# Optimization experiments

Hardware: AMD Instinct MI355X
Metric: run time of the kernel (lower is better)

Reference implementation:

```python
import jax, jax.numpy as jnp
import numpy as np

N = 10000      # nodes
DEG = 32       # avg degree
D_IN = 256     # in_feats
H = 128        # hidden_layers[0] == hidden_layers[2]
K = 3          # hidden_layers[1] = Chebyshev order
D_OUT = 64     # out_feat


def setup_inputs() -> dict:
    key = jax.random.key(0)
    ks = jax.random.split(key, 8)
    x = jax.random.normal(ks[0], (N, D_IN), jnp.float32)
    # sparse binary adjacency built by scattering into a dense [N, N] matrix
    src = jax.random.randint(ks[1], (N * DEG,), 0, N)
    dst = jax.random.randint(ks[2], (N * DEG,), 0, N)
    adj = jnp.zeros((N, N), jnp.float32).at[src, dst].set(1.0)
    init = lambda k, shape, fan: jax.random.normal(k, shape, jnp.float32) / np.sqrt(fan)
    W_in = init(ks[3], (D_IN, H), D_IN)
    b_in = jnp.zeros((H,), jnp.float32)
    W_cheb = init(ks[4], (K * H, H), K * H)   # dgl ChebConv: Linear(k*in, out)
    b_cheb = jnp.zeros((H,), jnp.float32)
    W_out = init(ks[5], (H, D_OUT), H)
    b_out = jnp.zeros((D_OUT,), jnp.float32)
    return dict(x=x, adj=adj, W_in=W_in, b_in=b_in, W_cheb=W_cheb,
                b_cheb=b_cheb, W_out=W_out, b_out=b_out)


def reference(x, adj, W_in, b_in, W_cheb, b_cheb, W_out, b_out):
    n = x.shape[0]
    # graph construction from dense adjacency (eager, like adj.to_dense().nonzero())
    src, dst = jnp.nonzero(adj)
    # symmetric normalization on in-degrees (dgl ChebConv, norm clamped at 1)
    deg = jax.ops.segment_sum(jnp.ones(src.shape[0], jnp.float32), dst, num_segments=n)
    norm = jnp.clip(deg, 1.0) ** -0.5  # [n]
    re_norm = 2.0 / 2.0  # lambda_max = [2] -> re_norm = 1

    def prop(h):
        # D^{-1/2} A D^{-1/2} h : gather at src, scatter-add at dst
        return jax.ops.segment_sum((h * norm[:, None])[src], dst, num_segments=n) * norm[:, None]

    # input linear + relu
    h = jax.nn.relu(x @ W_in + b_in)
    # Chebyshev recursion (dgl ChebConv with lambda_max=2)
    X0 = h
    X1 = -re_norm * prop(X0) + (re_norm - 1.0) * X0
    Xs = [X0, X1]
    Xpp, Xp = X0, X1
    for _ in range(2, K):
        Xi = -2.0 * re_norm * prop(Xp) + 2.0 * (re_norm - 1.0) * Xp - Xpp
        Xs.append(Xi)
        Xpp, Xp = Xp, Xi
    hc = jax.nn.relu(jnp.concatenate(Xs, axis=1) @ W_cheb + b_cheb)  # [n, H]
    return hc @ W_out + b_out  # [n, D_OUT]
```

## Files before the change

### kernel.cpp

```cpp
#include <hip/hip_runtime.h>
#include <hip/hip_bf16.h>
#include <cstdint>
#include <cstddef>

#define NN 10000
#define MAXDEG 128
#define LDX 384

#define GEMM_BLKS 313
#define CONV_BLK  1
#define SCAN_BLKS 3072
#define FAT_BLKS  (GEMM_BLKS + CONV_BLK + SCAN_BLKS)

typedef __attribute__((ext_vector_type(8))) short bf16x8;
typedef __attribute__((ext_vector_type(4))) float f32x4;

__device__ __forceinline__ float bf2f(unsigned short u) {
    union { unsigned int i; float f; } c; c.i = ((unsigned int)u) << 16; return c.f;
}
__device__ __forceinline__ unsigned short f2bf(float f) {
    union { float f; unsigned int i; } c; c.f = f;
    unsigned int x = c.i;
    return (unsigned short)((x + 0x7fffu + ((x >> 16) & 1u)) >> 16);
}

__global__ __launch_bounds__(256) void fat_scan_gemm(
        const float4* __restrict__ adj4, int total4,
        int* __restrict__ cnt, int* __restrict__ csr,
        const float* __restrict__ x, const float* __restrict__ W_in,
        const float* __restrict__ b_in,
        const float* __restrict__ W_cheb, const float* __restrict__ W_out,
        unsigned short* __restrict__ Xc,
        unsigned short* __restrict__ Wtc, unsigned short* __restrict__ Wto) {
    __shared__ float smem[10240];
    int bid = blockIdx.x;
    int t = threadIdx.x;

    if (bid < GEMM_BLKS) {
        constexpr int K = 256, N = 128, BM = 32, KC = 64;
        float* Wl = smem;
        float* Al = smem + KC * N;
        int r0 = bid * BM;
        int c2 = t & 63;
        int g  = t >> 6;
        float2 acc[8];
        #pragma unroll
        for (int i = 0; i < 8; ++i) acc[i] = make_float2(0.f, 0.f);

        for (int kk = 0; kk < K; kk += KC) {
            __syncthreads();
            #pragma unroll
            for (int i = 0; i < KC * N / 4 / 256; ++i) {
                int idx = t + i * 256;
                ((float4*)Wl)[idx] = ((const float4*)(W_in + (size_t)kk * N))[idx];
            }
            #pragma unroll
            for (int i = 0; i < BM * KC / 4 / 256; ++i) {
                int idx = t + i * 256;
                int row = idx >> 4;
                int cf  = idx & 15;
                float4 v = make_float4(0.f, 0.f, 0.f, 0.f);
                if (r0 + row < NN)
                    v = *(const float4*)(x + (size_t)(r0 + row) * K + kk + cf * 4);
                *(float4*)(Al + row * KC + cf * 4) = v;
            }
            __syncthreads();
            for (int k = 0; k < KC; k += 4) {
                float4 av[8];
                #pragma unroll
                for (int rr = 0; rr < 8; ++rr)
                    av[rr] = *(const float4*)(Al + (g * 8 + rr) * KC + k);
                #pragma unroll
                for (int k2 = 0; k2 < 4; ++k2) {
                    float2 wv = *(const float2*)(Wl + (k + k2) * N + c2 * 2);
                    #pragma unroll
                    for (int rr = 0; rr < 8; ++rr) {
                        float a = (k2 == 0) ? av[rr].x : (k2 == 1) ? av[rr].y
                                  : (k2 == 2) ? av[rr].z : av[rr].w;
                        acc[rr].x = fmaf(a, wv.x, acc[rr].x);
                        acc[rr].y = fmaf(a, wv.y, acc[rr].y);
                    }
                }
            }
        }
        float2 bv = *(const float2*)(b_in + c2 * 2);
        #pragma unroll
        for (int rr = 0; rr < 8; ++rr) {
            int r = r0 + g * 8 + rr;
            if (r < NN) {
                float vx = fmaxf(acc[rr].x + bv.x, 0.f);
                float vy = fmaxf(acc[rr].y + bv.y, 0.f);
                uint32_t o = (uint32_t)f2bf(vx) | ((uint32_t)f2bf(vy) << 16);
                *(uint32_t*)(Xc + (size_t)r * LDX + c2 * 2) = o;
            }
        }
    } else if (bid == GEMM_BLKS) {
        for (int idx = t; idx < 384 * 128; idx += 256) {
            int k = idx >> 7, c = idx & 127;
            Wtc[c * 384 + k] = f2bf(W_cheb[idx]);
        }
        for (int idx = t; idx < 128 * 64; idx += 256) {
            int k = idx >> 6, c = idx & 63;
            Wto[c * 128 + k] = f2bf(W_out[idx]);
        }
    } else {
        int sid = bid - (GEMM_BLKS + CONV_BLK);
        int idx = sid * 256 + t;
        int stride = SCAN_BLKS * 256;
        for (int p = idx; p < total4; p += stride) {
            float4 v = adj4[p];
            if (v.x != 0.f || v.y != 0.f || v.z != 0.f || v.w != 0.f) {
                int lin = p * 4;
                #pragma unroll
                for (int c = 0; c < 4; ++c) {
                    float f = (c == 0) ? v.x : (c == 1) ? v.y : (c == 2) ? v.z : v.w;
                    if (f != 0.f) {
                        int l = lin + c;
                        int i = l / NN;
                        int j = l - i * NN;
                        int pos = atomicAdd(&cnt[j], 1);
                        if (pos < MAXDEG) csr[j * MAXDEG + pos] = i;
                    }
                }
            }
        }
    }
}

template<bool SUB>
__global__ __launch_bounds__(256) void prop_k(unsigned short* __restrict__ X,
                                              const int* __restrict__ csr,
                                              const int* __restrict__ cnt,
                                              int srcOff, int dstOff, float scale) {
    int j = blockIdx.x * 4 + (threadIdx.x >> 6);
    if (j >= NN) return;
    int lane = threadIdx.x & 63;
    int cj = cnt[j];
    int cn = min(cj, MAXDEG);
    const int* nb = csr + j * MAXDEG;
    float ax0 = 0.f, ay0 = 0.f, ax1 = 0.f, ay1 = 0.f;
    int e = 0;
    for (; e + 2 <= cn; e += 2) {
        int i0 = nb[e], i1 = nb[e + 1];
        int c0 = cnt[i0], c1 = cnt[i1];
        uint32_t h0 = *(const uint32_t*)(X + (size_t)i0 * LDX + srcOff + lane * 2);
        uint32_t h1 = *(const uint32_t*)(X + (size_t)i1 * LDX + srcOff + lane * 2);
        float w0 = rsqrtf(fmaxf((float)c0, 1.f));
        float w1 = rsqrtf(fmaxf((float)c1, 1.f));
        ax0 = fmaf(w0, bf2f((unsigned short)h0), ax0);
        ay0 = fmaf(w0, bf2f((unsigned short)(h0 >> 16)), ay0);
        ax1 = fmaf(w1, bf2f((unsigned short)h1), ax1);
        ay1 = fmaf(w1, bf2f((unsigned short)(h1 >> 16)), ay1);
    }
    if (e < cn) {
        int i0 = nb[e];
        float w0 = rsqrtf(fmaxf((float)cnt[i0], 1.f));
        uint32_t h0 = *(const uint32_t*)(X + (size_t)i0 * LDX + srcOff + lane * 2);
        ax0 = fmaf(w0, bf2f((unsigned short)h0), ax0);
        ay0 = fmaf(w0, bf2f((unsigned short)(h0 >> 16)), ay0);
    }
    float s = scale * rsqrtf(fmaxf((float)cj, 1.f));
    float rx = s * (ax0 + ax1), ry = s * (ay0 + ay1);
    if (SUB) {
        uint32_t x0 = *(const uint32_t*)(X + (size_t)j * LDX + lane * 2);
        rx -= bf2f((unsigned short)x0);
        ry -= bf2f((unsigned short)(x0 >> 16));
    }
    uint32_t o = (uint32_t)f2bf(rx) | ((uint32_t)f2bf(ry) << 16);
    *(uint32_t*)(X + (size_t)j * LDX + dstOff + lane * 2) = o;
}

__global__ __launch_bounds__(256) void cheb_out_mfma(
        const unsigned short* __restrict__ Xc,
        const unsigned short* __restrict__ Wtc,
        const float* __restrict__ bc,
        const unsigned short* __restrict__ Wto,
        const float* __restrict__ bo,
        float* __restrict__ out) {
    __shared__ unsigned short hcL[32][136];
    int t = threadIdx.x;
    int w = t >> 6, lane = t & 63;
    int r0 = blockIdx.x * 32;
    int lr = lane & 15;
    int kg = lane >> 4;

    f32x4 acc[2][2] = {};
    for (int k0 = 0; k0 < 384; k0 += 32) {
        bf16x8 a[2], b[2];
        #pragma unroll
        for (int m = 0; m < 2; ++m) {
            int row = r0 + m * 16 + lr;
            row = min(row, NN - 1);
            a[m] = *(const bf16x8*)(Xc + (size_t)row * LDX + k0 + kg * 8);
        }
        #pragma unroll
        for (int n = 0; n < 2; ++n) {
            int col = w * 32 + n * 16 + lr;
            b[n] = *(const bf16x8*)(Wtc + (size_t)col * 384 + k0 + kg * 8);
        }
        #pragma unroll
        for (int m = 0; m < 2; ++m)
            #pragma unroll
            for (int n = 0; n < 2; ++n)
                acc[m][n] = __builtin_amdgcn_mfma_f32_16x16x32_bf16(a[m], b[n], acc[m][n], 0, 0, 0);
    }
    #pragma unroll
    for (int m = 0; m < 2; ++m) {
        #pragma unroll
        for (int n = 0; n < 2; ++n) {
            int col = w * 32 + n * 16 + lr;
            float bv = bc[col];
            #pragma unroll
            for (int r = 0; r < 4; ++r) {
                int row = m * 16 + kg * 4 + r;
                hcL[row][col] = f2bf(fmaxf(acc[m][n][r] + bv, 0.f));
            }
        }
    }
    __syncthreads();
    int rt = w >> 1, ch = w & 1;
    f32x4 a2[2] = {};
    for (int k0 = 0; k0 < 128; k0 += 32) {
        bf16x8 af = *(const bf16x8*)(&hcL[rt * 16 + lr][k0 + kg * 8]);
        #pragma unroll
        for (int n = 0; n < 2; ++n) {
            int col = ch * 32 + n * 16 + lr;
            bf16x8 bf_ = *(const bf16x8*)(Wto + (size_t)col * 128 + k0 + kg * 8);
            a2[n] = __builtin_amdgcn_mfma_f32_16x16x32_bf16(af, bf_, a2[n], 0, 0, 0);
        }
    }
    #pragma unroll
    for (int n = 0; n < 2; ++n) {
        int col = ch * 32 + n * 16 + lr;
        float bv = bo[col];
        #pragma unroll
        for (int r = 0; r < 4; ++r) {
            int row = r0 + rt * 16 + kg * 4 + r;
            if (row < NN) out[(size_t)row * 64 + col] = a2[n][r] + bv;
        }
    }
}

extern "C" void kernel_launch(void* const* d_in, const int* in_sizes, int n_in,
                              void* d_out, int out_size, void* d_ws, size_t ws_size,
                              hipStream_t stream) {
    const float* x      = (const float*)d_in[0];
    const float* adj    = (const float*)d_in[1];
    const float* W_in   = (const float*)d_in[2];
    const float* b_in   = (const float*)d_in[3];
    const float* W_cheb = (const float*)d_in[4];
    const float* b_cheb = (const float*)d_in[5];
    const float* W_out  = (const float*)d_in[6];
    const float* b_out  = (const float*)d_in[7];
    float* out = (float*)d_out;

    char* ws = (char*)d_ws;
    int*            cnt = (int*)(ws + 0);
    int*            csr = (int*)(ws + 40960);
    unsigned short* Xc  = (unsigned short*)(ws + 5160960);
    unsigned short* Wtc = (unsigned short*)(ws + 12845056);
    unsigned short* Wto = (unsigned short*)(ws + 12943360);

    int adj_total = in_sizes[1];

    hipMemsetAsync(cnt, 0, NN * sizeof(int), stream);
    fat_scan_gemm<<<FAT_BLKS, 256, 0, stream>>>(
        (const float4*)adj, adj_total / 4, cnt, csr,
        x, W_in, b_in, W_cheb, W_out, Xc, Wtc, Wto);
    prop_k<false><<<(NN + 3) / 4, 256, 0, stream>>>(Xc, csr, cnt, 0, 128, -1.0f);
    prop_k<true><<<(NN + 3) / 4, 256, 0, stream>>>(Xc, csr, cnt, 128, 256, -2.0f);
    cheb_out_mfma<<<(NN + 31) / 32, 256, 0, stream>>>(Xc, Wtc, b_cheb, Wto, b_out, out);
}
```

Before: 238.5 us.

## Replace atomic adjacency scan with column-blocked scan plus prefix-sum stitch

The dense adjacency is now scanned in 80-row by 4-column tiles. Each thread records nonzero row indices into fixed-size per-segment buckets with no atomics, so the global atomicAdd per edge and the memset are gone. A new stitch kernel prefix-sums the per-block counts with wave shuffles, writes an ordered CSR, and precomputes the rsqrt degree norms. prop_k then reads those norms instead of recomputing them from counts, and is unrolled to 4 neighbours per step. The cost is an extra kernel launch and intermediate buffers. Segments are capped at 12 entries, so a column with more than 12 nonzeros inside one 80-row block silently drops edges.

```diff
diff --git a/kernel.cpp b/kernel.cpp
--- a/kernel.cpp
+++ b/kernel.cpp
@@ -7,10 +7,12 @@
 #define MAXDEG 128
 #define LDX 384
 
+#define COLSCAN_BLKS 1250
+#define RB_ROWS 80
+#define NRB 125
+#define SEG2 12
 #define GEMM_BLKS 313
-#define CONV_BLK  1
-#define SCAN_BLKS 3072
-#define FAT_BLKS  (GEMM_BLKS + CONV_BLK + SCAN_BLKS)
+#define FATG (COLSCAN_BLKS + GEMM_BLKS + 1)
 
 typedef __attribute__((ext_vector_type(8))) short bf16x8;
 typedef __attribute__((ext_vector_type(4))) float f32x4;
@@ -24,23 +26,55 @@
     return (unsigned short)((x + 0x7fffu + ((x >> 16) & 1u)) >> 16);
 }
 
-__global__ __launch_bounds__(256) void fat_scan_gemm(
-        const float4* __restrict__ adj4, int total4,
-        int* __restrict__ cnt, int* __restrict__ csr,
+__global__ __launch_bounds__(256) void fat_colscan_gemm(
+        const float* __restrict__ A,
+        int* __restrict__ csr2,
+        int* __restrict__ cnt2,
         const float* __restrict__ x, const float* __restrict__ W_in,
         const float* __restrict__ b_in,
         const float* __restrict__ W_cheb, const float* __restrict__ W_out,
         unsigned short* __restrict__ Xc,
         unsigned short* __restrict__ Wtc, unsigned short* __restrict__ Wto) {
-    __shared__ float smem[10240];
+    __shared__ float smem[5120];
     int bid = blockIdx.x;
     int t = threadIdx.x;
 
-    if (bid < GEMM_BLKS) {
-        constexpr int K = 256, N = 128, BM = 32, KC = 64;
+    if (bid < COLSCAN_BLKS) {
+        if (t >= 250) return;
+        int rb  = bid / 10;
+        int cbs = bid % 10;
+        int r0  = rb * RB_ROWS;
+        int c   = cbs * 1000 + t * 4;
+        const float4* base = (const float4*)A;
+        int idx0 = r0 * (NN / 4) + (c >> 2);
+
+        float4 buf[8];
+        #pragma unroll
+        for (int d = 0; d < 8; ++d)
+            buf[d] = base[idx0 + d * (NN / 4)];
+
+        int n0 = 0, n1 = 0, n2 = 0, n3 = 0;
+        size_t segbase = ((size_t)rb * NN + c) * SEG2;
+
+        #pragma unroll 8
+        for (int r = 0; r < RB_ROWS; ++r) {
+            float4 v = buf[r & 7];
+            buf[r & 7] = base[idx0 + min(r + 8, RB_ROWS - 1) * (NN / 4)];
+            int row = r0 + r;
+            if (v.x != 0.f) { if (n0 < SEG2) csr2[segbase + n0] = row; n0++; }
+            if (v.y != 0.f) { if (n1 < SEG2) csr2[segbase + SEG2 + n1] = row; n1++; }
+            if (v.z != 0.f) { if (n2 < SEG2) csr2[segbase + 2 * SEG2 + n2] = row; n2++; }
+            if (v.w != 0.f) { if (n3 < SEG2) csr2[segbase + 3 * SEG2 + n3] = row; n3++; }
+        }
+        cnt2[(c + 0) * 128 + rb] = n0;
+        cnt2[(c + 1) * 128 + rb] = n1;
+        cnt2[(c + 2) * 128 + rb] = n2;
+        cnt2[(c + 3) * 128 + rb] = n3;
+    } else if (bid < COLSCAN_BLKS + GEMM_BLKS) {
+        constexpr int K = 256, N = 128, BM = 32, KC = 32;
         float* Wl = smem;
         float* Al = smem + KC * N;
-        int r0 = bid * BM;
+        int r0 = (bid - COLSCAN_BLKS) * BM;
         int c2 = t & 63;
         int g  = t >> 6;
         float2 acc[8];
@@ -54,11 +88,9 @@
                 int idx = t + i * 256;
                 ((float4*)Wl)[idx] = ((const float4*)(W_in + (size_t)kk * N))[idx];
             }
-            #pragma unroll
-            for (int i = 0; i < BM * KC / 4 / 256; ++i) {
-                int idx = t + i * 256;
-                int row = idx >> 4;
-                int cf  = idx & 15;
+            {
+                int row = t >> 3;
+                int cf  = t & 7;
                 float4 v = make_float4(0.f, 0.f, 0.f, 0.f);
                 if (r0 + row < NN)
                     v = *(const float4*)(x + (size_t)(r0 + row) * K + kk + cf * 4);
@@ -94,7 +126,7 @@
                 *(uint32_t*)(Xc + (size_t)r * LDX + c2 * 2) = o;
             }
         }
-    } else if (bid == GEMM_BLKS) {
+    } else {
         for (int idx = t; idx < 384 * 128; idx += 256) {
             int k = idx >> 7, c = idx & 127;
             Wtc[c * 384 + k] = f2bf(W_cheb[idx]);
@@ -103,27 +135,46 @@
             int k = idx >> 6, c = idx & 63;
             Wto[c * 128 + k] = f2bf(W_out[idx]);
         }
-    } else {
-        int sid = bid - (GEMM_BLKS + CONV_BLK);
-        int idx = sid * 256 + t;
-        int stride = SCAN_BLKS * 256;
-        for (int p = idx; p < total4; p += stride) {
-            float4 v = adj4[p];
-            if (v.x != 0.f || v.y != 0.f || v.z != 0.f || v.w != 0.f) {
-                int lin = p * 4;
-                #pragma unroll
-                for (int c = 0; c < 4; ++c) {
-                    float f = (c == 0) ? v.x : (c == 1) ? v.y : (c == 2) ? v.z : v.w;
-                    if (f != 0.f) {
-                        int l = lin + c;
-                        int i = l / NN;
-                        int j = l - i * NN;
-                        int pos = atomicAdd(&cnt[j], 1);
-                        if (pos < MAXDEG) csr[j * MAXDEG + pos] = i;
-                    }
-                }
-            }
-        }
+    }
+}
+
+__global__ __launch_bounds__(256) void stitch_norm(
+        const int* __restrict__ csr2, const int* __restrict__ cnt2,
+        int* __restrict__ csr, int* __restrict__ cnt, float* __restrict__ nrm) {
+    int w = threadIdx.x >> 6, l = threadIdx.x & 63;
+    int c = blockIdx.x * 4 + w;
+    if (c >= NN) return;
+
+    int a  = (l < NRB)      ? cnt2[c * 128 + l]      : 0;
+    int bb = (l + 64 < NRB) ? cnt2[c * 128 + 64 + l] : 0;
+
+    int xa = a, xb = bb;
+    #pragma unroll
+    for (int d = 1; d < 64; d <<= 1) {
+        int ya = __shfl_up(xa, d);
+        int yb = __shfl_up(xb, d);
+        if (l >= d) { xa += ya; xb += yb; }
+    }
+    int totalA = __shfl(xa, 63);
+    int total  = totalA + __shfl(xb, 63);
+    int offA = xa - a;
+    int offB = totalA + xb - bb;
+
+    const int* segA = csr2 + ((size_t)l * NN + c) * SEG2;
+    for (int e = 0; e < a; ++e) {
+        int o = offA + e;
+        if (o < MAXDEG) csr[(size_t)c * MAXDEG + o] = segA[e];
+    }
+    if (l + 64 < NRB) {
+        const int* segB = csr2 + ((size_t)(l + 64) * NN + c) * SEG2;
+        for (int e = 0; e < bb; ++e) {
+            int o = offB + e;
+            if (o < MAXDEG) csr[(size_t)c * MAXDEG + o] = segB[e];
+        }
+    }
+    if (l == 0) {
+        cnt[c] = min(total, MAXDEG);
+        nrm[c] = rsqrtf(fmaxf((float)total, 1.f));
     }
 }
 
@@ -131,36 +182,42 @@
 __global__ __launch_bounds__(256) void prop_k(unsigned short* __restrict__ X,
                                               const int* __restrict__ csr,
                                               const int* __restrict__ cnt,
+                                              const float* __restrict__ nrm,
                                               int srcOff, int dstOff, float scale) {
     int j = blockIdx.x * 4 + (threadIdx.x >> 6);
     if (j >= NN) return;
     int lane = threadIdx.x & 63;
-    int cj = cnt[j];
-    int cn = min(cj, MAXDEG);
-    const int* nb = csr + j * MAXDEG;
+    int cn = cnt[j];
+    const int* nb = csr + (size_t)j * MAXDEG;
     float ax0 = 0.f, ay0 = 0.f, ax1 = 0.f, ay1 = 0.f;
+    float ax2 = 0.f, ay2 = 0.f, ax3 = 0.f, ay3 = 0.f;
     int e = 0;
-    for (; e + 2 <= cn; e += 2) {
-        int i0 = nb[e], i1 = nb[e + 1];
-        int c0 = cnt[i0], c1 = cnt[i1];
+    for (; e + 4 <= cn; e += 4) {
+        int i0 = nb[e], i1 = nb[e + 1], i2 = nb[e + 2], i3 = nb[e + 3];
+        float w0 = nrm[i0], w1 = nrm[i1], w2 = nrm[i2], w3 = nrm[i3];
         uint32_t h0 = *(const uint32_t*)(X + (size_t)i0 * LDX + srcOff + lane * 2);
         uint32_t h1 = *(const uint32_t*)(X + (size_t)i1 * LDX + srcOff + lane * 2);
-        float w0 = rsqrtf(fmaxf((float)c0, 1.f));
-        float w1 = rsqrtf(fmaxf((float)c1, 1.f));
+        uint32_t h2 = *(const uint32_t*)(X + (size_t)i2 * LDX + srcOff + lane * 2);
+        uint32_t h3 = *(const uint32_t*)(X + (size_t)i3 * LDX + srcOff + lane * 2);
         ax0 = fmaf(w0, bf2f((unsigned short)h0), ax0);
         ay0 = fmaf(w0, bf2f((unsigned short)(h0 >> 16)), ay0);
         ax1 = fmaf(w1, bf2f((unsigned short)h1), ax1);
         ay1 = fmaf(w1, bf2f((unsigned short)(h1 >> 16)), ay1);
-    }
-    if (e < cn) {
+        ax2 = fmaf(w2, bf2f((unsigned short)h2), ax2);
+        ay2 = fmaf(w2, bf2f((unsigned short)(h2 >> 16)), ay2);
+        ax3 = fmaf(w3, bf2f((unsigned short)h3), ax3);
+        ay3 = fmaf(w3, bf2f((unsigned short)(h3 >> 16)), ay3);
+    }
+    for (; e < cn; ++e) {
         int i0 = nb[e];
-        float w0 = rsqrtf(fmaxf((float)cnt[i0], 1.f));
+        float w0 = nrm[i0];
         uint32_t h0 = *(const uint32_t*)(X + (size_t)i0 * LDX + srcOff + lane * 2);
         ax0 = fmaf(w0, bf2f((unsigned short)h0), ax0);
         ay0 = fmaf(w0, bf2f((unsigned short)(h0 >> 16)), ay0);
     }
-    float s = scale * rsqrtf(fmaxf((float)cj, 1.f));
-    float rx = s * (ax0 + ax1), ry = s * (ay0 + ay1);
+    float s = scale * nrm[j];
+    float rx = s * ((ax0 + ax1) + (ax2 + ax3));
+    float ry = s * ((ay0 + ay1) + (ay2 + ay3));
     if (SUB) {
         uint32_t x0 = *(const uint32_t*)(X + (size_t)j * LDX + lane * 2);
         rx -= bf2f((unsigned short)x0);
@@ -255,19 +312,19 @@
     float* out = (float*)d_out;
 
     char* ws = (char*)d_ws;
-    int*            cnt = (int*)(ws + 0);
-    int*            csr = (int*)(ws + 40960);
-    unsigned short* Xc  = (unsigned short*)(ws + 5160960);
-    unsigned short* Wtc = (unsigned short*)(ws + 12845056);
-    unsigned short* Wto = (unsigned short*)(ws + 12943360);
-
-    int adj_total = in_sizes[1];
-
-    hipMemsetAsync(cnt, 0, NN * sizeof(int), stream);
-    fat_scan_gemm<<<FAT_BLKS, 256, 0, stream>>>(
-        (const float4*)adj, adj_total / 4, cnt, csr,
-        x, W_in, b_in, W_cheb, W_out, Xc, Wtc, Wto);
-    prop_k<false><<<(NN + 3) / 4, 256, 0, stream>>>(Xc, csr, cnt, 0, 128, -1.0f);
-    prop_k<true><<<(NN + 3) / 4, 256, 0, stream>>>(Xc, csr, cnt, 128, 256, -2.0f);
+    int*            cnt  = (int*)(ws + 0);
+    float*          nrm  = (float*)(ws + 65536);
+    int*            csr  = (int*)(ws + 131072);
+    int*            cnt2 = (int*)(ws + 5308416);
+    unsigned short* Xc   = (unsigned short*)(ws + 10485760);
+    unsigned short* Wtc  = (unsigned short*)(ws + 18874368);
+    unsigned short* Wto  = (unsigned short*)(ws + 19005440);
+    int*            csr2 = (int*)(ws + 20971520);
+
+    fat_colscan_gemm<<<FATG, 256, 0, stream>>>(
+        adj, csr2, cnt2, x, W_in, b_in, W_cheb, W_out, Xc, Wtc, Wto);
+    stitch_norm<<<2500, 256, 0, stream>>>(csr2, cnt2, csr, cnt, nrm);
+    prop_k<false><<<(NN + 3) / 4, 256, 0, stream>>>(Xc, csr, cnt, nrm, 0, 128, -1.0f);
+    prop_k<true><<<(NN + 3) / 4, 256, 0, stream>>>(Xc, csr, cnt, nrm, 128, 256, -2.0f);
     cheb_out_mfma<<<(NN + 31) / 32, 256, 0, stream>>>(Xc, Wtc, b_cheb, Wto, b_out, out);
 }
```

After: 234.5 us. About the same (-1.7%).
